# Kernel optimization log

Hardware: AMD Instinct MI355X
Metric: run time of the kernel (lower is better)

## Reference

```python
import jax, jax.numpy as jnp
import numpy as np
from jax import lax

T, B, D = 1024, 32, 1024


def setup_inputs() -> dict:
    key = jax.random.key(0)
    k1, k2, k3, k4 = jax.random.split(key, 4)
    xav = (6.0 / (D + D)) ** 0.5  # xavier_uniform bound
    return {
        "x": jax.random.normal(k1, (T, B, D), dtype=jnp.float32),
        "h0": jnp.zeros((B, D), dtype=jnp.float32),
        "W_alpha": jax.random.uniform(k2, (D, D), minval=-xav, maxval=xav, dtype=jnp.float32),
        "d_alpha": jnp.full((D,), 0.1, dtype=jnp.float32),
        "b_alpha": jnp.full((D,), 2.0, dtype=jnp.float32),
        "W_x": jax.random.uniform(k3, (D, D), minval=-xav, maxval=xav, dtype=jnp.float32),
        "b_v": jnp.zeros((D,), dtype=jnp.float32),
    }


def reference(x, h0, W_alpha, d_alpha, b_alpha, W_x, b_v):
    # Precompute batched GEMMs once (x_t @ W.T), as in the original.
    alpha_x = jnp.einsum("tbd,ed->tbe", x, W_alpha)          # [T,B,D]
    v = jnp.tanh(jnp.einsum("tbd,ed->tbe", x, W_x) + b_v)    # [T,B,D]

    def step(h_prev, inp):
        ax_t, v_t = inp
        alpha = jax.nn.sigmoid(ax_t + d_alpha * h_prev + b_alpha)
        h_new = alpha * h_prev + (1.0 - alpha) * v_t
        out = h_new * h_new * jax.nn.sigmoid(h_new)  # h * silu(h)
        return h_new, (h_new, out)

    _, (hs, outs) = lax.scan(step, h0, (alpha_x, v))
    h = jnp.concatenate([h0[None], hs], axis=0)  # [T+1,B,D]
    return outs, h
```

## Files before the change

### kernel.cpp

```cpp
#include <hip/hip_runtime.h>
#include <hip/hip_bf16.h>
#include <stdint.h>

#define TT 1024
#define BB 32
#define DD 1024
#define MROWS (TT*BB)
#define NCOLS (2*DD)
#define KDIM  (DD)
#define SS (BB*DD)

typedef __attribute__((ext_vector_type(8))) short short8;
typedef __attribute__((ext_vector_type(4))) float f32x4;

__device__ __forceinline__ float bf2f(uint16_t u){
  union { uint32_t u; float f; } c; c.u = ((uint32_t)u) << 16; return c.f;
}
__device__ __forceinline__ uint16_t f2bf(float f){
  union { float f; uint32_t u; } c; c.f = f;
  uint32_t u = c.u;
  u += 0x7FFFu + ((u >> 16) & 1u);
  return (uint16_t)(u >> 16);
}
__device__ __forceinline__ float tanh_fast(float x){
  return 1.f - 2.f/(1.f + __expf(2.f*x));
}
__device__ __forceinline__ float sigmoid_fast(float x){
  return __builtin_amdgcn_rcpf(1.f + __expf(-x));
}

__global__ __launch_bounds__(256) void cvt_w_kernel(const float* __restrict__ Wa,
                                                    const float* __restrict__ Wx,
                                                    uint16_t* __restrict__ wc){
  int i = blockIdx.x * 256 + threadIdx.x;
  const int c    = i >> 8;
  const int col4 = i & 255;
  const int e = ((c >> 5) << 4) | (c & 15);
  const int s = (c >> 4) & 1;
  const float* src = (s ? Wx : Wa) + (size_t)e*DD + col4*4;
  float4 f = *(const float4*)src;
  ushort4 o;
  o.x = f2bf(f.x); o.y = f2bf(f.y); o.z = f2bf(f.z); o.w = f2bf(f.w);
  ((ushort4*)wc)[i] = o;
}

__global__ __launch_bounds__(512, 2) void gemm_dual(const float* __restrict__ x,
                                                    const uint16_t* __restrict__ wc,
                                                    const float* __restrict__ bv,
                                                    uint32_t* __restrict__ av){
  __shared__ __align__(16) uint16_t lds[49152];
  char* ldsc = (char*)lds;

  const int tid  = threadIdx.x;
  const int lane = tid & 63;
  const int w    = tid >> 6;
  const int wm   = w >> 2;
  const int wn   = w & 3;
  const int fr   = lane & 15;
  const int fq   = lane >> 4;

  const int bid = blockIdx.x;
  const int bsw = (bid & 7) * 128 + (bid >> 3);
  const int bm  = (bsw >> 3) << 8;
  const int bn  = (bsw & 7) << 8;

  f32x4 acc[8][4] = {};

  const int lslot = (tid & 3) ^ ((tid >> 3) & 3);

  #define STAGE_B(kt, bufb, u) { \
    const uint16_t* g_ = wc + (size_t)(bn + (u)*128 + (tid >> 2))*KDIM + (kt)*32 + lslot*8; \
    char* d_ = ldsc + (bufb) + 16384 + (u)*8192 + w*1024; \
    __builtin_amdgcn_global_load_lds((const __attribute__((address_space(1))) void*)g_, \
                                     (__attribute__((address_space(3))) void*)d_, 16, 0, 0); \
  }

  float4 a0lo, a0hi, a1lo, a1hi;
  #define LOAD_A(kt) { \
    const float* g0_ = x + (size_t)(bm + (tid >> 2))*KDIM + (kt)*32 + lslot*8; \
    a0lo = *(const float4*)g0_; a0hi = *(const float4*)(g0_ + 4); \
    const float* g1_ = g0_ + (size_t)128*KDIM; \
    a1lo = *(const float4*)g1_; a1hi = *(const float4*)(g1_ + 4); \
  }
  #define WRITE_A(bufb) { \
    union { short8 v; __hip_bfloat162 b[4]; } P0_, P1_; \
    P0_.b[0] = __float22bfloat162_rn(make_float2(a0lo.x, a0lo.y)); \
    P0_.b[1] = __float22bfloat162_rn(make_float2(a0lo.z, a0lo.w)); \
    P0_.b[2] = __float22bfloat162_rn(make_float2(a0hi.x, a0hi.y)); \
    P0_.b[3] = __float22bfloat162_rn(make_float2(a0hi.z, a0hi.w)); \
    P1_.b[0] = __float22bfloat162_rn(make_float2(a1lo.x, a1lo.y)); \
    P1_.b[1] = __float22bfloat162_rn(make_float2(a1lo.z, a1lo.w)); \
    P1_.b[2] = __float22bfloat162_rn(make_float2(a1hi.x, a1hi.y)); \
    P1_.b[3] = __float22bfloat162_rn(make_float2(a1hi.z, a1hi.w)); \
    char* d0_ = ldsc + (bufb) + (tid >> 2)*64 + (tid & 3)*16; \
    *(short8*)d0_ = P0_.v; \
    *(short8*)(d0_ + 8192) = P1_.v; \
  }
  #define WALL asm volatile("" ::: "memory");

  const int slotoff = (fq ^ ((fr >> 1) & 3)) * 16;
  const int aoff0 = (wm*128 + fr)*64 + slotoff;
  const int boff0 = 16384 + (wn*64 + fr)*64 + slotoff;

  LOAD_A(0) WALL
  STAGE_B(0, 0, 0) STAGE_B(0, 0, 1) WALL
  asm volatile("s_waitcnt vmcnt(2)" ::: "memory");
  WRITE_A(0)
  LOAD_A(1) WALL
  STAGE_B(1, 32768, 0) STAGE_B(1, 32768, 1)
  asm volatile("s_waitcnt vmcnt(6)" ::: "memory");
  asm volatile("s_waitcnt lgkmcnt(0)" ::: "memory");
  __builtin_amdgcn_s_barrier();

  int bR = 0;
  for (int t = 0; t < 32; ++t){
    const int bRb  = bR * 32768;
    const int bW1b = ((bR == 2) ? 0 : bR + 1) * 32768;
    const int bW2b = ((bR == 0) ? 2 : bR - 1) * 32768;

    if (t < 31){
      asm volatile("s_waitcnt vmcnt(2)" ::: "memory");
      WRITE_A(bW1b)
    }

    short8 aF[4], bF[4], aG[4];
    #pragma unroll
    for (int m = 0; m < 4; ++m)
      aF[m] = *(const short8*)(ldsc + bRb + aoff0 + m*1024);
    #pragma unroll
    for (int n = 0; n < 4; ++n)
      bF[n] = *(const short8*)(ldsc + bRb + boff0 + n*1024);
    if (t < 30){ LOAD_A(t+2) WALL STAGE_B(t+2, bW2b, 0) STAGE_B(t+2, bW2b, 1) }

    #pragma unroll
    for (int m = 0; m < 4; ++m)
      #pragma unroll
      for (int n = 0; n < 4; ++n)
        acc[m][n] = __builtin_amdgcn_mfma_f32_16x16x32_bf16(aF[m], bF[n], acc[m][n], 0, 0, 0);

    #pragma unroll
    for (int m = 0; m < 4; ++m)
      aG[m] = *(const short8*)(ldsc + bRb + aoff0 + 4096 + m*1024);

    #pragma unroll
    for (int m = 0; m < 4; ++m)
      #pragma unroll
      for (int n = 0; n < 4; ++n)
        acc[4+m][n] = __builtin_amdgcn_mfma_f32_16x16x32_bf16(aG[m], bF[n], acc[4+m][n], 0, 0, 0);

    if (t < 30){
      asm volatile("s_waitcnt vmcnt(6)" ::: "memory");
    } else if (t == 30){
      asm volatile("s_waitcnt vmcnt(0)" ::: "memory");
    }
    if (t < 31){
      asm volatile("s_waitcnt lgkmcnt(0)" ::: "memory");
      __builtin_amdgcn_s_barrier();
    }

    bR = (bR == 2) ? 0 : bR + 1;
  }
  #undef STAGE_B
  #undef LOAD_A
  #undef WRITE_A
  #undef WALL

  const int ebase = (bn + wn*64) >> 1;
  const float bvn0 = bv[ebase + fr];
  const float bvn1 = bv[ebase + 16 + fr];
  #pragma unroll
  for (int m = 0; m < 8; ++m){
    #pragma unroll
    for (int j = 0; j < 4; ++j){
      const int row = bm + wm*128 + m*16 + fq*4 + j;
      const int tt = row >> 5, b = row & 31;
      const size_t base = (size_t)tt*SS + (size_t)b*DD;
      const float a0  = acc[m][0][j];
      const float vt0 = tanh_fast(acc[m][1][j] + bvn0);
      av[base + ebase + fr] = (uint32_t)f2bf(a0) | ((uint32_t)f2bf(vt0) << 16);
      const float a1  = acc[m][2][j];
      const float vt1 = tanh_fast(acc[m][3][j] + bvn1);
      av[base + ebase + 16 + fr] = (uint32_t)f2bf(a1) | ((uint32_t)f2bf(vt1) << 16);
    }
  }
}

#define SCAN_STEP(u, tcur)                                        \
  {                                                               \
    const float a_ = bf2f((uint16_t)(u));                         \
    const float v_ = bf2f((uint16_t)((u) >> 16));                 \
    const float al_ = sigmoid_fast(a_ + da*h + ba);               \
    h = al_*(h - v_) + v_;                                        \
    const float sg_ = sigmoid_fast(h);                            \
    __builtin_nontemporal_store(h*h*sg_, &outs[(size_t)(tcur)*SS + idx]); \
    __builtin_nontemporal_store(h, &houts[(size_t)((tcur)+1)*SS + idx]);  \
  }

__global__ __launch_bounds__(64) void scan_kernel(const uint32_t* __restrict__ av,
                                                  const float* __restrict__ h0,
                                                  const float* __restrict__ d_alpha,
                                                  const float* __restrict__ b_alpha,
                                                  float* __restrict__ outs,
                                                  float* __restrict__ houts){
  const int idx = blockIdx.x * 64 + threadIdx.x;
  const int e = idx & (DD-1);
  const float da = d_alpha[e];
  const float ba = b_alpha[e];
  float h = h0[idx];
  __builtin_nontemporal_store(h, &houts[idx]);

  uint32_t bufA[32], bufB[32];
  #pragma unroll
  for (int j = 0; j < 32; ++j) bufA[j] = av[(size_t)j*SS + idx];

  for (int t0 = 0; t0 < TT; t0 += 64){
    #pragma unroll
    for (int j = 0; j < 32; ++j) bufB[j] = av[(size_t)(t0+32+j)*SS + idx];
    #pragma unroll
    for (int j = 0; j < 32; ++j) SCAN_STEP(bufA[j], t0 + j);
    if (t0 + 64 < TT){
      #pragma unroll
      for (int j = 0; j < 32; ++j) bufA[j] = av[(size_t)(t0+64+j)*SS + idx];
    }
    #pragma unroll
    for (int j = 0; j < 32; ++j) SCAN_STEP(bufB[j], t0 + 32 + j);
  }
}

extern "C" void kernel_launch(void* const* d_in, const int* in_sizes, int n_in,
                              void* d_out, int out_size, void* d_ws, size_t ws_size,
                              hipStream_t stream){
  const float* x  = (const float*)d_in[0];
  const float* h0 = (const float*)d_in[1];
  const float* Wa = (const float*)d_in[2];
  const float* da = (const float*)d_in[3];
  const float* ba = (const float*)d_in[4];
  const float* Wx = (const float*)d_in[5];
  const float* bv = (const float*)d_in[6];

  float* outs  = (float*)d_out;
  float* houts = outs + (size_t)TT*BB*DD;

  uint8_t* ws = (uint8_t*)d_ws;
  uint16_t* wcb = (uint16_t*)ws;
  uint32_t* av  = (uint32_t*)(ws + (size_t)NCOLS*KDIM*2);

  hipLaunchKernelGGL(cvt_w_kernel, dim3(2048), dim3(256), 0, stream, Wa, Wx, wcb);
  hipLaunchKernelGGL(gemm_dual, dim3((NCOLS/256)*(MROWS/256)), dim3(512), 0, stream,
                     x, wcb, bv, av);
  hipLaunchKernelGGL(scan_kernel, dim3(SS/64), dim3(64), 0, stream,
                     av, h0, da, ba, outs, houts);
}
```

Baseline: 259.5 us.

## Double-buffer A-tile registers to prefetch two K-steps ahead in GEMM

The fp32 A-tile global loads now alternate between two register sets, so two K-steps of A are in flight at once. The bf16 conversion and LDS write of the next tile move to the end of each iteration, after the MFMAs, instead of stalling at the top. This is meant to hide global load latency behind the matrix math. The cost is 16 more VGPRs, which adds register pressure, and a manual 2x unroll of the K loop.

```diff
diff --git a/kernel.cpp b/kernel.cpp
--- a/kernel.cpp
+++ b/kernel.cpp
@@ -75,23 +75,23 @@
                                      (__attribute__((address_space(3))) void*)d_, 16, 0, 0); \
   }
 
-  float4 a0lo, a0hi, a1lo, a1hi;
-  #define LOAD_A(kt) { \
+  float4 ax0, ax1, ax2, ax3, ay0, ay1, ay2, ay3;
+  #define LOAD_A(kt, r0, r1, r2, r3) { \
     const float* g0_ = x + (size_t)(bm + (tid >> 2))*KDIM + (kt)*32 + lslot*8; \
-    a0lo = *(const float4*)g0_; a0hi = *(const float4*)(g0_ + 4); \
+    r0 = *(const float4*)g0_; r1 = *(const float4*)(g0_ + 4); \
     const float* g1_ = g0_ + (size_t)128*KDIM; \
-    a1lo = *(const float4*)g1_; a1hi = *(const float4*)(g1_ + 4); \
-  }
-  #define WRITE_A(bufb) { \
+    r2 = *(const float4*)g1_; r3 = *(const float4*)(g1_ + 4); \
+  }
+  #define WRITE_A(bufb, r0, r1, r2, r3) { \
     union { short8 v; __hip_bfloat162 b[4]; } P0_, P1_; \
-    P0_.b[0] = __float22bfloat162_rn(make_float2(a0lo.x, a0lo.y)); \
-    P0_.b[1] = __float22bfloat162_rn(make_float2(a0lo.z, a0lo.w)); \
-    P0_.b[2] = __float22bfloat162_rn(make_float2(a0hi.x, a0hi.y)); \
-    P0_.b[3] = __float22bfloat162_rn(make_float2(a0hi.z, a0hi.w)); \
-    P1_.b[0] = __float22bfloat162_rn(make_float2(a1lo.x, a1lo.y)); \
-    P1_.b[1] = __float22bfloat162_rn(make_float2(a1lo.z, a1lo.w)); \
-    P1_.b[2] = __float22bfloat162_rn(make_float2(a1hi.x, a1hi.y)); \
-    P1_.b[3] = __float22bfloat162_rn(make_float2(a1hi.z, a1hi.w)); \
+    P0_.b[0] = __float22bfloat162_rn(make_float2(r0.x, r0.y)); \
+    P0_.b[1] = __float22bfloat162_rn(make_float2(r0.z, r0.w)); \
+    P0_.b[2] = __float22bfloat162_rn(make_float2(r1.x, r1.y)); \
+    P0_.b[3] = __float22bfloat162_rn(make_float2(r1.z, r1.w)); \
+    P1_.b[0] = __float22bfloat162_rn(make_float2(r2.x, r2.y)); \
+    P1_.b[1] = __float22bfloat162_rn(make_float2(r2.z, r2.w)); \
+    P1_.b[2] = __float22bfloat162_rn(make_float2(r3.x, r3.y)); \
+    P1_.b[3] = __float22bfloat162_rn(make_float2(r3.z, r3.w)); \
     char* d0_ = ldsc + (bufb) + (tid >> 2)*64 + (tid & 3)*16; \
     *(short8*)d0_ = P0_.v; \
     *(short8*)(d0_ + 8192) = P1_.v; \
@@ -102,64 +102,66 @@
   const int aoff0 = (wm*128 + fr)*64 + slotoff;
   const int boff0 = 16384 + (wn*64 + fr)*64 + slotoff;
 
-  LOAD_A(0) WALL
+  LOAD_A(0, ax0, ax1, ax2, ax3) WALL
   STAGE_B(0, 0, 0) STAGE_B(0, 0, 1) WALL
-  asm volatile("s_waitcnt vmcnt(2)" ::: "memory");
-  WRITE_A(0)
-  LOAD_A(1) WALL
+  LOAD_A(1, ay0, ay1, ay2, ay3) WALL
   STAGE_B(1, 32768, 0) STAGE_B(1, 32768, 1)
+  asm volatile("s_waitcnt vmcnt(8)" ::: "memory");
+  WRITE_A(0, ax0, ax1, ax2, ax3)
   asm volatile("s_waitcnt vmcnt(6)" ::: "memory");
   asm volatile("s_waitcnt lgkmcnt(0)" ::: "memory");
   __builtin_amdgcn_s_barrier();
 
+  #define TILE_BODY(t, LR0,LR1,LR2,LR3, WR0,WR1,WR2,WR3) { \
+    const int bRb  = bR * 32768; \
+    const int bW1b = ((bR == 2) ? 0 : bR + 1) * 32768; \
+    const int bW2b = ((bR == 0) ? 2 : bR - 1) * 32768; \
+    short8 aF[4], bF[4], aG[4]; \
+    _Pragma("unroll") \
+    for (int m = 0; m < 4; ++m) \
+      aF[m] = *(const short8*)(ldsc + bRb + aoff0 + m*1024); \
+    _Pragma("unroll") \
+    for (int n = 0; n < 4; ++n) \
+      bF[n] = *(const short8*)(ldsc + bRb + boff0 + n*1024); \
+    if ((t) < 30){ LOAD_A((t)+2, LR0,LR1,LR2,LR3) WALL STAGE_B((t)+2, bW2b, 0) STAGE_B((t)+2, bW2b, 1) } \
+    _Pragma("unroll") \
+    for (int m = 0; m < 4; ++m) \
+      _Pragma("unroll") \
+      for (int n = 0; n < 4; ++n) \
+        acc[m][n] = __builtin_amdgcn_mfma_f32_16x16x32_bf16(aF[m], bF[n], acc[m][n], 0, 0, 0); \
+    _Pragma("unroll") \
+    for (int m = 0; m < 4; ++m) \
+      aG[m] = *(const short8*)(ldsc + bRb + aoff0 + 4096 + m*1024); \
+    _Pragma("unroll") \
+    for (int m = 0; m < 4; ++m) \
+      _Pragma("unroll") \
+      for (int n = 0; n < 4; ++n) \
+        acc[4+m][n] = __builtin_amdgcn_mfma_f32_16x16x32_bf16(aG[m], bF[n], acc[4+m][n], 0, 0, 0); \
+    if ((t) < 30){ \
+      asm volatile("s_waitcnt vmcnt(8)" ::: "memory");    \
+      WRITE_A(bW1b, WR0,WR1,WR2,WR3) \
+      asm volatile("s_waitcnt vmcnt(6)" ::: "memory");    \
+      asm volatile("s_waitcnt lgkmcnt(0)" ::: "memory"); \
+      __builtin_amdgcn_s_barrier(); \
+    } else if ((t) == 30){ \
+      asm volatile("s_waitcnt vmcnt(2)" ::: "memory");    \
+      WRITE_A(bW1b, WR0,WR1,WR2,WR3) \
+      asm volatile("s_waitcnt vmcnt(0)" ::: "memory");    \
+      asm volatile("s_waitcnt lgkmcnt(0)" ::: "memory"); \
+      __builtin_amdgcn_s_barrier(); \
+    } \
+    bR = (bR == 2) ? 0 : bR + 1; \
+  }
+
   int bR = 0;
-  for (int t = 0; t < 32; ++t){
-    const int bRb  = bR * 32768;
-    const int bW1b = ((bR == 2) ? 0 : bR + 1) * 32768;
-    const int bW2b = ((bR == 0) ? 2 : bR - 1) * 32768;
-
-    if (t < 31){
-      asm volatile("s_waitcnt vmcnt(2)" ::: "memory");
-      WRITE_A(bW1b)
-    }
-
-    short8 aF[4], bF[4], aG[4];
-    #pragma unroll
-    for (int m = 0; m < 4; ++m)
-      aF[m] = *(const short8*)(ldsc + bRb + aoff0 + m*1024);
-    #pragma unroll
-    for (int n = 0; n < 4; ++n)
-      bF[n] = *(const short8*)(ldsc + bRb + boff0 + n*1024);
-    if (t < 30){ LOAD_A(t+2) WALL STAGE_B(t+2, bW2b, 0) STAGE_B(t+2, bW2b, 1) }
-
-    #pragma unroll
-    for (int m = 0; m < 4; ++m)
-      #pragma unroll
-      for (int n = 0; n < 4; ++n)
-        acc[m][n] = __builtin_amdgcn_mfma_f32_16x16x32_bf16(aF[m], bF[n], acc[m][n], 0, 0, 0);
-
-    #pragma unroll
-    for (int m = 0; m < 4; ++m)
-      aG[m] = *(const short8*)(ldsc + bRb + aoff0 + 4096 + m*1024);
-
-    #pragma unroll
-    for (int m = 0; m < 4; ++m)
-      #pragma unroll
-      for (int n = 0; n < 4; ++n)
-        acc[4+m][n] = __builtin_amdgcn_mfma_f32_16x16x32_bf16(aG[m], bF[n], acc[4+m][n], 0, 0, 0);
-
-    if (t < 30){
-      asm volatile("s_waitcnt vmcnt(6)" ::: "memory");
-    } else if (t == 30){
-      asm volatile("s_waitcnt vmcnt(0)" ::: "memory");
-    }
-    if (t < 31){
-      asm volatile("s_waitcnt lgkmcnt(0)" ::: "memory");
-      __builtin_amdgcn_s_barrier();
-    }
-
-    bR = (bR == 2) ? 0 : bR + 1;
-  }
+  #pragma unroll 1
+  for (int tp = 0; tp < 16; ++tp){
+    const int te = 2*tp;
+    TILE_BODY(te, ax0,ax1,ax2,ax3, ay0,ay1,ay2,ay3)
+    const int to = 2*tp + 1;
+    TILE_BODY(to, ay0,ay1,ay2,ay3, ax0,ax1,ax2,ax3)
+  }
+  #undef TILE_BODY
   #undef STAGE_B
   #undef LOAD_A
   #undef WRITE_A
```

New measurement: 277.8 us. +7.1%, slower.
